# Kernel optimization log

Hardware: AMD Instinct MI355X
Metric: run time of the kernel (lower is better)

## Reference

```python
import jax, jax.numpy as jnp
import numpy as np

N = 20000
E = 640000
IN_CH = 256
HID = 128
OUT_CH = 64
HEADS = 8
C1 = HID // HEADS   # 16 per-head dim, layer 1 (concat)
C2 = OUT_CH         # 64 per-head dim, layer 2 (head mean)
NEG_SLOPE = 0.2


def gat_conv(x, edge_index, W, a_src, a_dst, b, concat):
    """PyG GATConv (no self loops, eval mode / no dropout).
    W: [F_in, H*C], a_src/a_dst: [H, C], b: [H*C] or [C]."""
    H, C = a_src.shape
    h = (x @ W).reshape(-1, H, C)                      # [N, H, C]
    s_src = jnp.einsum('nhc,hc->nh', h, a_src)         # [N, H]
    s_dst = jnp.einsum('nhc,hc->nh', h, a_dst)         # [N, H]
    src, dst = edge_index[0], edge_index[1]
    e = jax.nn.leaky_relu(s_src[src] + s_dst[dst], NEG_SLOPE)  # [E, H]
    # segment softmax over incoming edges of each destination node
    m = jax.ops.segment_max(e, dst, num_segments=N)    # [N, H] (-inf for isolated)
    p = jnp.exp(e - m[dst])                            # [E, H]
    z = jax.ops.segment_sum(p, dst, num_segments=N)    # [N, H]
    alpha = p / z[dst]                                 # [E, H]
    out = jax.ops.segment_sum(h[src] * alpha[..., None], dst, num_segments=N)  # [N,H,C]
    out = out.reshape(-1, H * C) if concat else out.mean(axis=1)
    return out + b


def hetero_layer(x, edge_indices, Ws, a_srcs, a_dsts, bs, concat):
    # HeteroConv(aggr='mean') over edge types targeting 'user'
    outs = [gat_conv(x, edge_indices[t], Ws[t], a_srcs[t], a_dsts[t], bs[t], concat)
            for t in range(len(edge_indices))]
    return sum(outs) / len(outs)


def setup_inputs() -> dict:
    key = jax.random.key(0)
    ks = jax.random.split(key, 16)
    g = 0.1
    return {
        'x': jax.random.normal(ks[0], (N, IN_CH), dtype=jnp.float32),
        'edge_index_a': jax.random.randint(ks[1], (2, E), 0, N, dtype=jnp.int32).astype(jnp.int64),
        'edge_index_b': jax.random.randint(ks[2], (2, E), 0, N, dtype=jnp.int32).astype(jnp.int64),
        # layer 1 params, stacked over 2 edge types
        'W1': jax.random.normal(ks[3], (2, IN_CH, HEADS * C1), dtype=jnp.float32) * g,
        'a1_src': jax.random.normal(ks[4], (2, HEADS, C1), dtype=jnp.float32) * g,
        'a1_dst': jax.random.normal(ks[5], (2, HEADS, C1), dtype=jnp.float32) * g,
        'b1': jnp.zeros((2, HEADS * C1), dtype=jnp.float32),
        # layer 2 params
        'W2': jax.random.normal(ks[6], (2, HID, HEADS * C2), dtype=jnp.float32) * g,
        'a2_src': jax.random.normal(ks[7], (2, HEADS, C2), dtype=jnp.float32) * g,
        'a2_dst': jax.random.normal(ks[8], (2, HEADS, C2), dtype=jnp.float32) * g,
        'b2': jnp.zeros((2, C2), dtype=jnp.float32),
        # classifier
        'Wc1': jax.random.normal(ks[9], (OUT_CH, 32), dtype=jnp.float32) * g,
        'bc1': jnp.zeros((32,), dtype=jnp.float32),
        'Wc2': jax.random.normal(ks[10], (32, 2), dtype=jnp.float32) * g,
        'bc2': jnp.zeros((2,), dtype=jnp.float32),
    }


def reference(x, edge_index_a, edge_index_b, W1, a1_src, a1_dst, b1,
              W2, a2_src, a2_dst, b2, Wc1, bc1, Wc2, bc2):
    eis = [edge_index_a, edge_index_b]
    h = hetero_layer(x, eis, W1, a1_src, a1_dst, b1, concat=True)   # [N, 128]
    h = jax.nn.elu(h)  # (dropout is identity in eval mode)
    h = hetero_layer(h, eis, W2, a2_src, a2_dst, b2, concat=False)  # [N, 64]
    h = jax.nn.elu(h)
    logits = jax.nn.relu(h @ Wc1 + bc1) @ Wc2 + bc2                 # [N, 2]
    return logits
```

## Files before the change

kernel.cpp:

```cpp
#include <hip/hip_runtime.h>
#include <hip/hip_bf16.h>
#include <math.h>

#define NN 20000
#define EE 640000
#define NB 157
#define BCAP 5120
#define NBLK 160
#define CHNK 4000

typedef float v2f __attribute__((ext_vector_type(2)));
typedef __attribute__((ext_vector_type(8))) short bf16x8;
typedef __attribute__((ext_vector_type(4))) float f32x4;

__device__ __forceinline__ void wave_fence() {
  __builtin_amdgcn_wave_barrier();
  asm volatile("s_waitcnt lgkmcnt(0)" ::: "memory");
  __builtin_amdgcn_wave_barrier();
}

__device__ __forceinline__ unsigned pack_bf2(float a, float b) {
  __hip_bfloat162 h2 = __float22bfloat162_rn(make_float2(a, b));
  return *(unsigned*)&h2;
}
__device__ __forceinline__ float2 unpack_bf2(unsigned v) {
  float2 r;
  unsigned lo = v << 16, hi = v & 0xffff0000u;
  r.x = __uint_as_float(lo);
  r.y = __uint_as_float(hi);
  return r;
}

__global__ __launch_bounds__(256) void bin_k(const int* __restrict__ ea,
                                             const int* __restrict__ eb,
                                             int* __restrict__ gcnt,
                                             int* __restrict__ bbuf) {
  int t = blockIdx.y;
  const int* ei = t ? eb : ea;
  int tid = threadIdx.x;
  __shared__ int lh[NB], lbase[NB];
  if (tid < NB) lh[tid] = 0;
  __syncthreads();
  int e0 = blockIdx.x * CHNK;
  int e1 = min(e0 + CHNK, EE);
  int myb[16], myr[16], myv[16];
#pragma unroll
  for (int i = 0; i < 16; ++i) {
    int e = e0 + tid + i * 256;
    if (e < e1) {
      int s = ei[e], d = ei[EE + e];
      int b = d >> 7;
      myb[i] = b;
      myv[i] = (s << 7) | (d & 127);
      myr[i] = atomicAdd(&lh[b], 1);
    } else {
      myb[i] = -1;
    }
  }
  __syncthreads();
  if (tid < NB) {
    int c = lh[tid];
    lbase[tid] = c ? atomicAdd(&gcnt[t * NB + tid], c) : 0;
  }
  __syncthreads();
#pragma unroll
  for (int i = 0; i < 16; ++i) {
    int b = myb[i];
    if (b >= 0) {
      int pos = lbase[b] + myr[i];
      if (pos < BCAP) bbuf[((size_t)t * NB + b) * BCAP + pos] = myv[i];
    }
  }
}

__global__ __launch_bounds__(512) void bscan_k(const int* __restrict__ gcnt,
                                               int* __restrict__ bstart) {
  __shared__ int buf[512];
  int tid = threadIdx.x;
  int t = tid >> 8, b = tid & 255;
  int val = (b < NB) ? gcnt[t * NB + b] : 0;
  buf[tid] = val;
  __syncthreads();
  for (int s = 1; s < 256; s <<= 1) {
    int x = ((tid & 255) >= s) ? buf[tid - s] : 0;
    __syncthreads();
    buf[tid] += x;
    __syncthreads();
  }
  if (b < NB) bstart[t * NB + b] = buf[tid] - val;
}

__global__ __launch_bounds__(256) void build_k(const int* __restrict__ gcnt,
                                               const int* __restrict__ bstart,
                                               const int* __restrict__ bbuf,
                                               int* __restrict__ rowptr,
                                               int* __restrict__ csr) {
  int b = blockIdx.x, t = blockIdx.y;
  int cnt = gcnt[t * NB + b];
  int start = bstart[t * NB + b];
  int n0 = b << 7;
  int nlocal = min(128, NN - n0);
  int tid = threadIdx.x;
  __shared__ int arr[128], lcur[128];
  if (tid < 128) arr[tid] = 0;
  __syncthreads();
  const int* ebuf = bbuf + ((size_t)t * NB + b) * BCAP;
  for (int i = tid; i < cnt; i += 256) atomicAdd(&arr[ebuf[i] & 127], 1);
  __syncthreads();
  int deg = (tid < 128) ? arr[tid] : 0;
  for (int s = 1; s < 128; s <<= 1) {
    int x = (tid < 128 && tid >= s) ? arr[tid - s] : 0;
    __syncthreads();
    if (tid < 128) arr[tid] += x;
    __syncthreads();
  }
  if (tid < nlocal) {
    int incl = arr[tid];
    rowptr[t * (NN + 1) + n0 + tid + 1] = start + incl;
    lcur[tid] = start + incl - deg;
  }
  if (b == 0 && tid == 0) rowptr[t * (NN + 1)] = 0;
  __syncthreads();
  for (int i = tid; i < cnt; i += 256) {
    int v = ebuf[i];
    int pos = atomicAdd(&lcur[v & 127], 1);
    csr[(size_t)t * EE + pos] = v >> 7;
  }
}

template <int NT, int BM, int BN, int BK, int TM, int TN>
__global__ __launch_bounds__(NT) void sgemm_k(const float* __restrict__ A,
                                              const float* __restrict__ B,
                                              float* __restrict__ C, int M, int N, int K,
                                              long long Abs, long long Bbs, long long Cbs,
                                              unsigned* __restrict__ Cb, long long Cbb) {
  A += blockIdx.z * Abs; B += blockIdx.z * Bbs; C += blockIdx.z * Cbs;
  if (Cb) Cb += blockIdx.z * Cbb;
  const int bm = blockIdx.x * BM, bn = blockIdx.y * BN;
  __shared__ float As[BK][BM + 4];
  __shared__ float Bs[BK][BN + 4];
  int tid = threadIdx.x;
  constexpr int TX = BN / TN;
  int tx = tid % TX, ty = tid / TX;
  float acc[TM][TN] = {};
  for (int k0 = 0; k0 < K; k0 += BK) {
#pragma unroll
    for (int i = 0; i < (BM * BK) / (NT * 4); ++i) {
      int idx = tid + i * NT;
      int row = idx / (BK / 4), kq = idx % (BK / 4);
      float4 v = make_float4(0.f, 0.f, 0.f, 0.f);
      int gr = bm + row;
      if (gr < M) v = *(const float4*)&A[(size_t)gr * K + k0 + kq * 4];
      As[kq * 4 + 0][row] = v.x; As[kq * 4 + 1][row] = v.y;
      As[kq * 4 + 2][row] = v.z; As[kq * 4 + 3][row] = v.w;
    }
#pragma unroll
    for (int i = 0; i < (BK * BN) / (NT * 4); ++i) {
      int idx = tid + i * NT;
      int row = idx / (BN / 4), cq = idx % (BN / 4);
      *(float4*)&Bs[row][cq * 4] = *(const float4*)&B[(size_t)(k0 + row) * N + bn + cq * 4];
    }
    __syncthreads();
#pragma unroll
    for (int k = 0; k < BK; ++k) {
      float a[TM], b[TN];
#pragma unroll
      for (int i = 0; i < TM; i += 4) *(float4*)&a[i] = *(float4*)&As[k][ty * TM + i];
#pragma unroll
      for (int j = 0; j < TN; j += 4) *(float4*)&b[j] = *(float4*)&Bs[k][tx * TN + j];
#pragma unroll
      for (int i = 0; i < TM; ++i)
#pragma unroll
        for (int j = 0; j < TN; ++j) acc[i][j] += a[i] * b[j];
    }
    __syncthreads();
  }
#pragma unroll
  for (int i = 0; i < TM; ++i) {
    int gr = bm + ty * TM + i;
    if (gr < M) {
#pragma unroll
      for (int j = 0; j < TN; j += 4)
        *(float4*)&C[(size_t)gr * N + bn + tx * TN + j] = *(float4*)&acc[i][j];
      if (Cb) {
#pragma unroll
        for (int j = 0; j < TN; j += 2)
          Cb[(size_t)gr * (N >> 1) + ((bn + tx * TN + j) >> 1)] = pack_bf2(acc[i][j], acc[i][j + 1]);
      }
    }
  }
}

template <int C>
__global__ void score_k(const float* __restrict__ hf, const float* __restrict__ as_,
                        const float* __restrict__ ad_, float* __restrict__ ss,
                        float* __restrict__ sd) {
  int idx = blockIdx.x * 256 + threadIdx.x;
  if (idx >= 2 * NN * 8) return;
  int t = idx / (NN * 8), r = idx % (NN * 8), n = r / 8, hh = r % 8;
  const int HC = 8 * C;
  const float* hrow = hf + (size_t)t * NN * HC + (size_t)n * HC + hh * C;
  const float* a1 = as_ + t * HC + hh * C;
  const float* a2 = ad_ + t * HC + hh * C;
  float s1 = 0.f, s2 = 0.f;
#pragma unroll
  for (int c = 0; c < C; c += 4) {
    float4 f = *(const float4*)&hrow[c];
    float4 u = *(const float4*)&a1[c];
    float4 w = *(const float4*)&a2[c];
    s1 += f.x * u.x + f.y * u.y + f.z * u.z + f.w * u.w;
    s2 += f.x * w.x + f.y * w.y + f.z * w.z + f.w * w.w;
  }
  ss[idx] = s1; sd[idx] = s2;
}

__device__ __forceinline__ float lrelu(float v) { return v > 0.f ? v : 0.2f * v; }

__global__ __launch_bounds__(256) void aggw1_k(const int* __restrict__ rowptr,
                                               const int* __restrict__ csr,
                                               const float* __restrict__ ssrc,
                                               const float* __restrict__ sdst,
                                               const unsigned* __restrict__ hb,
                                               float* __restrict__ out) {
  int t = blockIdx.y;
  rowptr += t * (NN + 1); csr += (size_t)t * EE;
  ssrc += (size_t)t * NN * 8; sdst += (size_t)t * NN * 8;
  hb += (size_t)t * NN * 64; out += (size_t)t * NN * 128;
  int tid = threadIdx.x, w = tid >> 6, lane = tid & 63;
  int n = blockIdx.x * 4 + w;
  int row = rowptr[n], end = rowptr[n + 1];
  __shared__ int sidx[4][64];
  __shared__ float sexp[4][64][8];
  float4 sda = *(const float4*)&sdst[(size_t)n * 8];
  float4 sdb = *(const float4*)&sdst[(size_t)n * 8 + 4];
  float za_x = 0.f, za_y = 0.f, za_z = 0.f, za_w = 0.f;
  float zb_x = 0.f, zb_y = 0.f, zb_z = 0.f, zb_w = 0.f;
  int hme = lane >> 3;
  v2f acc = {0.f, 0.f};
  for (int base = row; base < end; base += 64) {
    int cnt = min(64, end - base);
    if (lane < cnt) {
      int s = csr[base + lane];
      sidx[w][lane] = s;
      float4 pa = *(const float4*)&ssrc[(size_t)s * 8];
      float4 pb = *(const float4*)&ssrc[(size_t)s * 8 + 4];
      float4 ea, eb;
      ea.x = __expf(lrelu(pa.x + sda.x)); ea.y = __expf(lrelu(pa.y + sda.y));
      ea.z = __expf(lrelu(pa.z + sda.z)); ea.w = __expf(lrelu(pa.w + sda.w));
      eb.x = __expf(lrelu(pb.x + sdb.x)); eb.y = __expf(lrelu(pb.y + sdb.y));
      eb.z = __expf(lrelu(pb.z + sdb.z)); eb.w = __expf(lrelu(pb.w + sdb.w));
      za_x += ea.x; za_y += ea.y; za_z += ea.z; za_w += ea.w;
      zb_x += eb.x; zb_y += eb.y; zb_z += eb.z; zb_w += eb.w;
      *(float4*)&sexp[w][lane][0] = ea;
      *(float4*)&sexp[w][lane][4] = eb;
    }
    wave_fence();
    for (int e = 0; e < cnt; ++e) {
      int s = sidx[w][e];
      float a = sexp[w][e][hme];
      float2 vf = unpack_bf2(hb[(size_t)s * 64 + lane]);
      v2f v = {vf.x, vf.y};
      acc += a * v;
    }
    wave_fence();
  }
#pragma unroll
  for (int off = 32; off; off >>= 1) {
    za_x += __shfl_xor(za_x, off); za_y += __shfl_xor(za_y, off);
    za_z += __shfl_xor(za_z, off); za_w += __shfl_xor(za_w, off);
    zb_x += __shfl_xor(zb_x, off); zb_y += __shfl_xor(zb_y, off);
    zb_z += __shfl_xor(zb_z, off); zb_w += __shfl_xor(zb_w, off);
  }
  float zh[8] = {za_x, za_y, za_z, za_w, zb_x, zb_y, zb_z, zb_w};
  float z = zh[hme];
  float iz = z > 0.f ? 1.f / z : 0.f;
  *(float2*)&out[(size_t)n * 128 + lane * 2] = make_float2(acc.x * iz, acc.y * iz);
}

__global__ void combine1_k(const float* __restrict__ oa, const float* __restrict__ ob,
                           const float* __restrict__ b1, float* __restrict__ hmid,
                           unsigned* __restrict__ hmidb) {
  int idx = blockIdx.x * 256 + threadIdx.x;
  if (idx >= NN * 64) return;
  int n = idx >> 6, j2 = idx & 63, j = j2 * 2;
  float2 va = *(const float2*)&oa[(size_t)n * 128 + j];
  float2 vb = *(const float2*)&ob[(size_t)n * 128 + j];
  float vx = 0.5f * ((va.x + b1[j]) + (vb.x + b1[128 + j]));
  float vy = 0.5f * ((va.y + b1[j + 1]) + (vb.y + b1[128 + j + 1]));
  vx = vx > 0.f ? vx : (__expf(vx) - 1.f);
  vy = vy > 0.f ? vy : (__expf(vy) - 1.f);
  *(float2*)&hmid[(size_t)n * 128 + j] = make_float2(vx, vy);
  hmidb[idx] = pack_bf2(vx, vy);
}

__global__ void fold2_k(const float* __restrict__ W2, const float* __restrict__ a2s,
                        const float* __restrict__ a2d, float* __restrict__ wsf,
                        float* __restrict__ wdf) {
  int idx = blockIdx.x * 256 + threadIdx.x;
  if (idx >= 2048) return;
  int t = idx >> 10, r = idx & 1023, hh = r >> 7, k = r & 127;
  const float* wrow = W2 + (size_t)t * 65536 + (size_t)k * 512 + hh * 64;
  const float* as = a2s + t * 512 + hh * 64;
  const float* ad = a2d + t * 512 + hh * 64;
  float s1 = 0.f, s2 = 0.f;
  for (int c = 0; c < 64; ++c) { s1 += wrow[c] * as[c]; s2 += wrow[c] * ad[c]; }
  wsf[idx] = s1; wdf[idx] = s2;
}

__global__ void foldBT_k(const float* __restrict__ W2, unsigned* __restrict__ BTp) {
  int idx = blockIdx.x * 256 + threadIdx.x;
  if (idx >= 65536) return;
  int t = idx >> 15, r = idx & 32767, c = r >> 9, kw = r & 511;
  int K0 = kw * 2, K1 = K0 + 1;
  int hh0 = K0 >> 7, kk0 = K0 & 127;
  int hh1 = K1 >> 7, kk1 = K1 & 127;
  float v0 = 0.125f * W2[(size_t)t * 65536 + (size_t)kk0 * 512 + hh0 * 64 + c];
  float v1 = 0.125f * W2[(size_t)t * 65536 + (size_t)kk1 * 512 + hh1 * 64 + c];
  BTp[idx] = pack_bf2(v0, v1);
}

__global__ void score2_k(const float* __restrict__ hmid, const float* __restrict__ wsf,
                         const float* __restrict__ wdf, float* __restrict__ ss,
                         float* __restrict__ sdo) {
  int idx = blockIdx.x * 256 + threadIdx.x;
  if (idx >= NN * 8) return;
  int n = idx >> 3, hh = idx & 7;
  const float* hm = hmid + (size_t)n * 128;
  const float* w0s = wsf + (size_t)hh * 128;
  const float* w0d = wdf + (size_t)hh * 128;
  const float* w1s = wsf + (size_t)(8 + hh) * 128;
  const float* w1d = wdf + (size_t)(8 + hh) * 128;
  float s0s = 0.f, s0d = 0.f, s1s = 0.f, s1d = 0.f;
#pragma unroll
  for (int c = 0; c < 128; c += 4) {
    float4 f = *(const float4*)&hm[c];
    float4 a = *(const float4*)&w0s[c];
    float4 b = *(const float4*)&w0d[c];
    float4 u = *(const float4*)&w1s[c];
    float4 v = *(const float4*)&w1d[c];
    s0s += f.x * a.x + f.y * a.y + f.z * a.z + f.w * a.w;
    s0d += f.x * b.x + f.y * b.y + f.z * b.z + f.w * b.w;
    s1s += f.x * u.x + f.y * u.y + f.z * u.z + f.w * u.w;
    s1d += f.x * v.x + f.y * v.y + f.z * v.z + f.w * v.w;
  }
  ss[idx] = s0s; sdo[idx] = s0d;
  ss[NN * 8 + idx] = s1s; sdo[NN * 8 + idx] = s1d;
}

__global__ __launch_bounds__(256) void aggw2_k(const int* __restrict__ rowptr,
                                               const int* __restrict__ csr,
                                               const float* __restrict__ ssrc,
                                               const float* __restrict__ sdst,
                                               const unsigned* __restrict__ hmidb,
                                               unsigned* __restrict__ aggp) {
  int t = blockIdx.y;
  rowptr += t * (NN + 1); csr += (size_t)t * EE;
  ssrc += (size_t)t * NN * 8; sdst += (size_t)t * NN * 8;
  aggp += (size_t)t * NN * 512;
  int tid = threadIdx.x, w = tid >> 6, lane = tid & 63;
  int n = blockIdx.x * 4 + w;
  int row = rowptr[n], end = rowptr[n + 1];
  __shared__ int sidx[4][64];
  __shared__ float sexp[4][64][8];
  float4 sda = *(const float4*)&sdst[(size_t)n * 8];
  float4 sdb = *(const float4*)&sdst[(size_t)n * 8 + 4];
  float za_x = 0.f, za_y = 0.f, za_z = 0.f, za_w = 0.f;
  float zb_x = 0.f, zb_y = 0.f, zb_z = 0.f, zb_w = 0.f;
  v2f acc[8];
#pragma unroll
  for (int i = 0; i < 8; ++i) acc[i] = (v2f){0.f, 0.f};
  for (int base = row; base < end; base += 64) {
    int cnt = min(64, end - base);
    if (lane < cnt) {
      int s = csr[base + lane];
      sidx[w][lane] = s;
      float4 pa = *(const float4*)&ssrc[(size_t)s * 8];
      float4 pb = *(const float4*)&ssrc[(size_t)s * 8 + 4];
      float4 ea, eb;
      ea.x = __expf(lrelu(pa.x + sda.x)); ea.y = __expf(lrelu(pa.y + sda.y));
      ea.z = __expf(lrelu(pa.z + sda.z)); ea.w = __expf(lrelu(pa.w + sda.w));
      eb.x = __expf(lrelu(pb.x + sdb.x)); eb.y = __expf(lrelu(pb.y + sdb.y));
      eb.z = __expf(lrelu(pb.z + sdb.z)); eb.w = __expf(lrelu(pb.w + sdb.w));
      za_x += ea.x; za_y += ea.y; za_z += ea.z; za_w += ea.w;
      zb_x += eb.x; zb_y += eb.y; zb_z += eb.z; zb_w += eb.w;
      *(float4*)&sexp[w][lane][0] = ea;
      *(float4*)&sexp[w][lane][4] = eb;
    }
    wave_fence();
    for (int e = 0; e < cnt; ++e) {
      int s = sidx[w][e];
      unsigned uv = hmidb[(size_t)s * 64 + lane];
      float4 ea = *(const float4*)&sexp[w][e][0];
      float4 eb = *(const float4*)&sexp[w][e][4];
      float2 vf = unpack_bf2(uv);
      v2f v = {vf.x, vf.y};
      acc[0] += ea.x * v;
      acc[1] += ea.y * v;
      acc[2] += ea.z * v;
      acc[3] += ea.w * v;
      acc[4] += eb.x * v;
      acc[5] += eb.y * v;
      acc[6] += eb.z * v;
      acc[7] += eb.w * v;
    }
    wave_fence();
  }
#pragma unroll
  for (int off = 32; off; off >>= 1) {
    za_x += __shfl_xor(za_x, off); za_y += __shfl_xor(za_y, off);
    za_z += __shfl_xor(za_z, off); za_w += __shfl_xor(za_w, off);
    zb_x += __shfl_xor(zb_x, off); zb_y += __shfl_xor(zb_y, off);
    zb_z += __shfl_xor(zb_z, off); zb_w += __shfl_xor(zb_w, off);
  }
  float zh[8] = {za_x, za_y, za_z, za_w, zb_x, zb_y, zb_z, zb_w};
#pragma unroll
  for (int i = 0; i < 8; ++i) {
    float z = zh[i];
    float iz = z > 0.f ? 1.f / z : 0.f;
    aggp[(size_t)n * 512 + i * 64 + lane] = pack_bf2(acc[i].x * iz, acc[i].y * iz);
  }
}

__global__ __launch_bounds__(256) void gemm2_k(const unsigned* __restrict__ Ap,
                                               const unsigned* __restrict__ BT,
                                               const float* __restrict__ b2,
                                               float* __restrict__ feat) {
  int tid = threadIdx.x, w = tid >> 6, l = tid & 63;
  int lr = l & 15, lg = l >> 4;
  int rowbase = blockIdx.x * 64 + w * 16;
  int arow = rowbase + lr;
  if (arow > NN - 1) arow = NN - 1;
  f32x4 acc0 = {0.f, 0.f, 0.f, 0.f}, acc1 = acc0, acc2 = acc0, acc3 = acc0;
#pragma unroll
  for (int t = 0; t < 2; ++t) {
    const unsigned* ap = Ap + (size_t)t * NN * 512 + (size_t)arow * 512 + lg * 4;
    const unsigned* bp = BT + t * 32768 + lr * 512 + lg * 4;
    for (int kw = 0; kw < 512; kw += 16) {
      uint4 av = *(const uint4*)(ap + kw);
      uint4 bv0 = *(const uint4*)(bp + kw);
      uint4 bv1 = *(const uint4*)(bp + 16 * 512 + kw);
      uint4 bv2 = *(const uint4*)(bp + 32 * 512 + kw);
      uint4 bv3 = *(const uint4*)(bp + 48 * 512 + kw);
      bf16x8 af = *(const bf16x8*)&av;
      acc0 = __builtin_amdgcn_mfma_f32_16x16x32_bf16(af, *(const bf16x8*)&bv0, acc0, 0, 0, 0);
      acc1 = __builtin_amdgcn_mfma_f32_16x16x32_bf16(af, *(const bf16x8*)&bv1, acc1, 0, 0, 0);
      acc2 = __builtin_amdgcn_mfma_f32_16x16x32_bf16(af, *(const bf16x8*)&bv2, acc2, 0, 0, 0);
      acc3 = __builtin_amdgcn_mfma_f32_16x16x32_bf16(af, *(const bf16x8*)&bv3, acc3, 0, 0, 0);
    }
  }
  f32x4 accs[4] = {acc0, acc1, acc2, acc3};
#pragma unroll
  for (int ct = 0; ct < 4; ++ct) {
    int col = ct * 16 + lr;
    float bsum = b2[col] + b2[64 + col];
#pragma unroll
    for (int r = 0; r < 4; ++r) {
      int row = rowbase + lg * 4 + r;
      if (row < NN) {
        float v = 0.5f * (accs[ct][r] + bsum);
        v = v > 0.f ? v : (__expf(v) - 1.f);
        feat[(size_t)row * 64 + col] = v;
      }
    }
  }
}

__global__ __launch_bounds__(256) void cls_k(const float* __restrict__ feat,
                                             const float* __restrict__ Wc1,
                                             const float* __restrict__ bc1,
                                             const float* __restrict__ Wc2,
                                             const float* __restrict__ bc2,
                                             float* __restrict__ out) {
  __shared__ float w1[64 * 32];
  __shared__ float w2[64];
  __shared__ float b1s[32], b2s[2];
  __shared__ float fs[8 * 64];
  __shared__ float hs[8 * 32];
  int tid = threadIdx.x;
  for (int i = tid; i < 2048; i += 256) w1[i] = Wc1[i];
  if (tid < 64) w2[tid] = Wc2[tid];
  if (tid < 32) b1s[tid] = bc1[tid];
  if (tid < 2) b2s[tid] = bc2[tid];
  int nbase = blockIdx.x * 8;
  for (int i = tid; i < 512; i += 256) fs[i] = feat[(size_t)nbase * 64 + i];
  __syncthreads();
  int local = tid >> 5, tt = tid & 31;
  const float* f = fs + local * 64;
  float acc = b1s[tt];
#pragma unroll
  for (int c = 0; c < 64; ++c) acc += f[c] * w1[c * 32 + tt];
  hs[local * 32 + tt] = fmaxf(acc, 0.f);
  __syncthreads();
  if (tid < 16) {
    int l = tid >> 1, j = tid & 1;
    float o = b2s[j];
#pragma unroll
    for (int i = 0; i < 32; ++i) o += hs[l * 32 + i] * w2[i * 2 + j];
    out[(size_t)(nbase + l) * 2 + j] = o;
  }
}

extern "C" void kernel_launch(void* const* d_in, const int* in_sizes, int n_in,
                              void* d_out, int out_size, void* d_ws, size_t ws_size,
                              hipStream_t stream) {
  const float* x   = (const float*)d_in[0];
  const int* eia   = (const int*)d_in[1];
  const int* eib   = (const int*)d_in[2];
  const float* W1  = (const float*)d_in[3];
  const float* a1s = (const float*)d_in[4];
  const float* a1d = (const float*)d_in[5];
  const float* b1  = (const float*)d_in[6];
  const float* W2  = (const float*)d_in[7];
  const float* a2s = (const float*)d_in[8];
  const float* a2d = (const float*)d_in[9];
  const float* b2  = (const float*)d_in[10];
  const float* Wc1 = (const float*)d_in[11];
  const float* bc1 = (const float*)d_in[12];
  const float* Wc2 = (const float*)d_in[13];
  const float* bc2 = (const float*)d_in[14];
  float* out = (float*)d_out;

  char* ws = (char*)d_ws;
  size_t off = 0;
  auto alloc = [&](size_t bytes) -> char* {
    char* p = ws + off;
    off += (bytes + 255) & ~(size_t)255;
    return p;
  };
  int* gcnt       = (int*)alloc((size_t)2 * NB * 4);
  int* bstart     = (int*)alloc((size_t)2 * NB * 4);
  int* bbuf       = (int*)alloc((size_t)2 * NB * BCAP * 4);
  int* rowptr     = (int*)alloc((size_t)2 * (NN + 1) * 4);
  int* csr        = (int*)alloc((size_t)2 * EE * 4);
  float* h1       = (float*)alloc((size_t)2 * NN * 128 * 4);
  unsigned* h1b   = (unsigned*)alloc((size_t)2 * NN * 64 * 4);
  float* s1s      = (float*)alloc((size_t)2 * NN * 8 * 4);
  float* s1d      = (float*)alloc((size_t)2 * NN * 8 * 4);
  float* o1       = (float*)alloc((size_t)2 * NN * 128 * 4);
  float* hmid     = (float*)alloc((size_t)NN * 128 * 4);
  unsigned* hmidb = (unsigned*)alloc((size_t)NN * 64 * 4);
  float* wsf      = (float*)alloc((size_t)2048 * 4);
  float* wdf      = (float*)alloc((size_t)2048 * 4);
  unsigned* BTp   = (unsigned*)alloc((size_t)65536 * 4);
  float* s2s      = (float*)alloc((size_t)2 * NN * 8 * 4);
  float* s2d      = (float*)alloc((size_t)2 * NN * 8 * 4);
  unsigned* aggp  = (unsigned*)alloc((size_t)2 * NN * 512 * 4);
  float* feat     = (float*)alloc((size_t)NN * 64 * 4);

  hipMemsetAsync(gcnt, 0, (size_t)2 * NB * 4, stream);
  bin_k<<<dim3(NBLK, 2), 256, 0, stream>>>(eia, eib, gcnt, bbuf);
  bscan_k<<<1, 512, 0, stream>>>(gcnt, bstart);
  build_k<<<dim3(NB, 2), 256, 0, stream>>>(gcnt, bstart, bbuf, rowptr, csr);

  fold2_k<<<8, 256, 0, stream>>>(W2, a2s, a2d, wsf, wdf);
  foldBT_k<<<256, 256, 0, stream>>>(W2, BTp);

  sgemm_k<256, 64, 64, 32, 4, 4><<<dim3((NN + 63) / 64, 2, 2), 256, 0, stream>>>(
      x, W1, h1, NN, 128, 256, 0LL, 256LL * 128, (long long)NN * 128, h1b, (long long)NN * 64);
  score_k<16><<<(2 * NN * 8 + 255) / 256, 256, 0, stream>>>(h1, a1s, a1d, s1s, s1d);
  aggw1_k<<<dim3(NN / 4, 2), 256, 0, stream>>>(rowptr, csr, s1s, s1d, h1b, o1);
  combine1_k<<<(NN * 64 + 255) / 256, 256, 0, stream>>>(o1, o1 + (size_t)NN * 128, b1, hmid, hmidb);

  score2_k<<<(NN * 8 + 255) / 256, 256, 0, stream>>>(hmid, wsf, wdf, s2s, s2d);
  aggw2_k<<<dim3(NN / 4, 2), 256, 0, stream>>>(rowptr, csr, s2s, s2d, hmidb, aggp);
  gemm2_k<<<(NN + 63) / 64, 256, 0, stream>>>(aggp, BTp, b2, feat);

  cls_k<<<NN / 8, 256, 0, stream>>>(feat, Wc1, bc1, Wc2, bc2, out);
}
```

Before: 444.3 us.

## Use MFMA for attention-weighted neighbor aggregation in both GAT layers

Replaces the two scalar per-edge aggregation kernels with one templated kernel that handles 32 edges per chunk. It stores the bf16 attention weights and a transposed tile of gathered neighbor features in LDS, then accumulates with 16x16x32 bf16 MFMA instructions. The goal is to cut per-edge FMA and LDS-broadcast cost, most of all in layer 2 where each edge feeds all 8 heads. In exchange it adds LDS zeroing, transpose stores and extra LDS traffic, and it rounds the attention weights to bf16. Layer 1 computes all head combinations but keeps only the diagonal, so most of its MFMA work is wasted.

```diff
diff --git a/kernel.cpp b/kernel.cpp
--- a/kernel.cpp
+++ b/kernel.cpp
@@ -216,65 +216,142 @@
 
 __device__ __forceinline__ float lrelu(float v) { return v > 0.f ? v : 0.2f * v; }
 
-__global__ __launch_bounds__(256) void aggw1_k(const int* __restrict__ rowptr,
-                                               const int* __restrict__ csr,
-                                               const float* __restrict__ ssrc,
-                                               const float* __restrict__ sdst,
-                                               const unsigned* __restrict__ hb,
-                                               float* __restrict__ out) {
+template <int MODE>
+__global__ __launch_bounds__(256) void aggm_k(const int* __restrict__ rowptr,
+                                              const int* __restrict__ csr,
+                                              const float* __restrict__ ssrc,
+                                              const float* __restrict__ sdst,
+                                              const unsigned* __restrict__ vsrc,
+                                              float* __restrict__ out1,
+                                              unsigned* __restrict__ out2) {
   int t = blockIdx.y;
   rowptr += t * (NN + 1); csr += (size_t)t * EE;
   ssrc += (size_t)t * NN * 8; sdst += (size_t)t * NN * 8;
-  hb += (size_t)t * NN * 64; out += (size_t)t * NN * 128;
+  if (MODE == 0) {
+    out1 += (size_t)t * NN * 128;
+    vsrc += (size_t)t * NN * 64;
+  } else {
+    out2 += (size_t)t * NN * 512;
+  }
   int tid = threadIdx.x, w = tid >> 6, lane = tid & 63;
+  int lg = lane >> 4;
   int n = blockIdx.x * 4 + w;
   int row = rowptr[n], end = rowptr[n + 1];
-  __shared__ int sidx[4][64];
-  __shared__ float sexp[4][64][8];
+  __shared__ __align__(16) unsigned VTw[4][2176];
+  __shared__ __align__(16) unsigned short ET[4][640];
+  __shared__ __align__(16) int sidx[4][32];
+  for (int i = lane; i < 2176; i += 64) VTw[w][i] = 0;
+  for (int i = lane; i < 640; i += 64) ET[w][i] = 0;
+  if (lane < 32) sidx[w][lane] = 0;
   float4 sda = *(const float4*)&sdst[(size_t)n * 8];
   float4 sdb = *(const float4*)&sdst[(size_t)n * 8 + 4];
-  float za_x = 0.f, za_y = 0.f, za_z = 0.f, za_w = 0.f;
-  float zb_x = 0.f, zb_y = 0.f, zb_z = 0.f, zb_w = 0.f;
-  int hme = lane >> 3;
-  v2f acc = {0.f, 0.f};
-  for (int base = row; base < end; base += 64) {
-    int cnt = min(64, end - base);
-    if (lane < cnt) {
-      int s = csr[base + lane];
-      sidx[w][lane] = s;
-      float4 pa = *(const float4*)&ssrc[(size_t)s * 8];
-      float4 pb = *(const float4*)&ssrc[(size_t)s * 8 + 4];
-      float4 ea, eb;
-      ea.x = __expf(lrelu(pa.x + sda.x)); ea.y = __expf(lrelu(pa.y + sda.y));
-      ea.z = __expf(lrelu(pa.z + sda.z)); ea.w = __expf(lrelu(pa.w + sda.w));
-      eb.x = __expf(lrelu(pb.x + sdb.x)); eb.y = __expf(lrelu(pb.y + sdb.y));
-      eb.z = __expf(lrelu(pb.z + sdb.z)); eb.w = __expf(lrelu(pb.w + sdb.w));
-      za_x += ea.x; za_y += ea.y; za_z += ea.z; za_w += ea.w;
-      zb_x += eb.x; zb_y += eb.y; zb_z += eb.z; zb_w += eb.w;
-      *(float4*)&sexp[w][lane][0] = ea;
-      *(float4*)&sexp[w][lane][4] = eb;
+  float z[8];
+#pragma unroll
+  for (int i = 0; i < 8; ++i) z[i] = 0.f;
+  f32x4 acc[8];
+#pragma unroll
+  for (int i = 0; i < 8; ++i) acc[i] = (f32x4){0.f, 0.f, 0.f, 0.f};
+  unsigned* VTp = &VTw[w][0];
+  const unsigned lane4 = lane << 2;
+  const unsigned wr0 = (unsigned)(2 * lane) * 17u;
+  const char* hbc = (const char*)vsrc;
+  for (int base = row; base < end; base += 32) {
+    int cnt = min(32, end - base);
+    if (lane < 32) {
+      float4 ea = {0.f, 0.f, 0.f, 0.f}, eb = {0.f, 0.f, 0.f, 0.f};
+      if (lane < cnt) {
+        int s = csr[base + lane];
+        sidx[w][lane] = s << 8;
+        float4 pa = *(const float4*)&ssrc[(size_t)s * 8];
+        float4 pb = *(const float4*)&ssrc[(size_t)s * 8 + 4];
+        ea.x = __expf(lrelu(pa.x + sda.x)); ea.y = __expf(lrelu(pa.y + sda.y));
+        ea.z = __expf(lrelu(pa.z + sda.z)); ea.w = __expf(lrelu(pa.w + sda.w));
+        eb.x = __expf(lrelu(pb.x + sdb.x)); eb.y = __expf(lrelu(pb.y + sdb.y));
+        eb.z = __expf(lrelu(pb.z + sdb.z)); eb.w = __expf(lrelu(pb.w + sdb.w));
+      }
+      unsigned p0 = pack_bf2(ea.x, ea.y), p1 = pack_bf2(ea.z, ea.w);
+      unsigned p2 = pack_bf2(eb.x, eb.y), p3 = pack_bf2(eb.z, eb.w);
+      float2 q0 = unpack_bf2(p0), q1 = unpack_bf2(p1);
+      float2 q2 = unpack_bf2(p2), q3 = unpack_bf2(p3);
+      z[0] += q0.x; z[1] += q0.y; z[2] += q1.x; z[3] += q1.y;
+      z[4] += q2.x; z[5] += q2.y; z[6] += q3.x; z[7] += q3.y;
+      unsigned short* et = &ET[w][lane];
+      et[0]   = (unsigned short)p0;  et[40]  = (unsigned short)(p0 >> 16);
+      et[80]  = (unsigned short)p1;  et[120] = (unsigned short)(p1 >> 16);
+      et[160] = (unsigned short)p2;  et[200] = (unsigned short)(p2 >> 16);
+      et[240] = (unsigned short)p3;  et[280] = (unsigned short)(p3 >> 16);
     }
     wave_fence();
-    for (int e = 0; e < cnt; ++e) {
-      int s = sidx[w][e];
-      float a = sexp[w][e][hme];
-      float2 vf = unpack_bf2(hb[(size_t)s * 64 + lane]);
-      v2f v = {vf.x, vf.y};
-      acc += a * v;
+    for (int g = 0; g < cnt; g += 4) {
+      unsigned off[4];
+      *(int4*)&off[0] = *(const int4*)&sidx[w][g];
+      unsigned u0 = *(const unsigned*)(hbc + (off[0] | lane4));
+      unsigned u1 = *(const unsigned*)(hbc + (off[1] | lane4));
+      unsigned u2 = *(const unsigned*)(hbc + (off[2] | lane4));
+      unsigned u3 = *(const unsigned*)(hbc + (off[3] | lane4));
+      unsigned lo01 = (u0 & 0xffffu) | (u1 << 16);
+      unsigned lo23 = (u2 & 0xffffu) | (u3 << 16);
+      unsigned hi01 = (u0 >> 16) | (u1 & 0xffff0000u);
+      unsigned hi23 = (u2 >> 16) | (u3 & 0xffff0000u);
+      unsigned r0 = wr0 + (unsigned)(g >> 1);
+      VTp[r0] = lo01; VTp[r0 + 1] = lo23;
+      VTp[r0 + 17] = hi01; VTp[r0 + 18] = hi23;
     }
     wave_fence();
+    bf16x8 af = *(const bf16x8*)&ET[w][(lane & 15) * 40 + lg * 8];
+#pragma unroll
+    for (int ct = 0; ct < 8; ++ct) {
+      const unsigned* vp = VTp + (unsigned)((ct * 16 + (lane & 15)) * 17 + lg * 4);
+      uint4 bv = make_uint4(vp[0], vp[1], vp[2], vp[3]);
+      bf16x8 bf = *(const bf16x8*)&bv;
+      acc[ct] = __builtin_amdgcn_mfma_f32_16x16x32_bf16(af, bf, acc[ct], 0, 0, 0);
+    }
+    wave_fence();
   }
 #pragma unroll
   for (int off = 32; off; off >>= 1) {
-    za_x += __shfl_xor(za_x, off); za_y += __shfl_xor(za_y, off);
-    za_z += __shfl_xor(za_z, off); za_w += __shfl_xor(za_w, off);
-    zb_x += __shfl_xor(zb_x, off); zb_y += __shfl_xor(zb_y, off);
-    zb_z += __shfl_xor(zb_z, off); zb_w += __shfl_xor(zb_w, off);
-  }
-  float zh[8] = {za_x, za_y, za_z, za_w, zb_x, zb_y, zb_z, zb_w};
-  float z = zh[hme];
-  float iz = z > 0.f ? 1.f / z : 0.f;
-  *(float2*)&out[(size_t)n * 128 + lane * 2] = make_float2(acc.x * iz, acc.y * iz);
+#pragma unroll
+    for (int i = 0; i < 8; ++i) z[i] += __shfl_xor(z[i], off);
+  }
+  float iz[8];
+#pragma unroll
+  for (int i = 0; i < 8; ++i) iz[i] = z[i] > 0.f ? 1.f / z[i] : 0.f;
+  if (MODE == 0) {
+    int col = lane & 15;
+    if (lg == 0) {
+#pragma unroll
+      for (int q = 0; q < 4; ++q)
+        out1[(size_t)n * 128 + q * 16 + col] = acc[q][q] * iz[q];
+    } else if (lg == 1) {
+#pragma unroll
+      for (int q = 0; q < 4; ++q)
+        out1[(size_t)n * 128 + (4 + q) * 16 + col] = acc[4 + q][q] * iz[4 + q];
+    }
+  } else {
+    int colp = (lane & 15) >> 1;
+    bool wr = (lane & 1) == 0;
+    if (lg == 0) {
+#pragma unroll
+      for (int ct = 0; ct < 8; ++ct) {
+#pragma unroll
+        for (int r = 0; r < 4; ++r) {
+          float v = acc[ct][r] * iz[r];
+          float v2 = __shfl_xor(v, 1);
+          if (wr) out2[(size_t)n * 512 + r * 64 + ct * 8 + colp] = pack_bf2(v, v2);
+        }
+      }
+    } else if (lg == 1) {
+#pragma unroll
+      for (int ct = 0; ct < 8; ++ct) {
+#pragma unroll
+        for (int r = 0; r < 4; ++r) {
+          float v = acc[ct][r] * iz[4 + r];
+          float v2 = __shfl_xor(v, 1);
+          if (wr) out2[(size_t)n * 512 + (4 + r) * 64 + ct * 8 + colp] = pack_bf2(v, v2);
+        }
+      }
+    }
+  }
 }
 
 __global__ void combine1_k(const float* __restrict__ oa, const float* __restrict__ ob,
@@ -347,105 +424,31 @@
   ss[NN * 8 + idx] = s1s; sdo[NN * 8 + idx] = s1d;
 }
 
-__global__ __launch_bounds__(256) void aggw2_k(const int* __restrict__ rowptr,
-                                               const int* __restrict__ csr,
-                                               const float* __restrict__ ssrc,
-                                               const float* __restrict__ sdst,
-                                               const unsigned* __restrict__ hmidb,
-                                               unsigned* __restrict__ aggp) {
-  int t = blockIdx.y;
-  rowptr += t * (NN + 1); csr += (size_t)t * EE;
-  ssrc += (size_t)t * NN * 8; sdst += (size_t)t * NN * 8;
-  aggp += (size_t)t * NN * 512;
-  int tid = threadIdx.x, w = tid >> 6, lane = tid & 63;
-  int n = blockIdx.x * 4 + w;
-  int row = rowptr[n], end = rowptr[n + 1];
-  __shared__ int sidx[4][64];
-  __shared__ float sexp[4][64][8];
-  float4 sda = *(const float4*)&sdst[(size_t)n * 8];
-  float4 sdb = *(const float4*)&sdst[(size_t)n * 8 + 4];
-  float za_x = 0.f, za_y = 0.f, za_z = 0.f, za_w = 0.f;
-  float zb_x = 0.f, zb_y = 0.f, zb_z = 0.f, zb_w = 0.f;
-  v2f acc[8];
-#pragma unroll
-  for (int i = 0; i < 8; ++i) acc[i] = (v2f){0.f, 0.f};
-  for (int base = row; base < end; base += 64) {
-    int cnt = min(64, end - base);
-    if (lane < cnt) {
-      int s = csr[base + lane];
-      sidx[w][lane] = s;
-      float4 pa = *(const float4*)&ssrc[(size_t)s * 8];
-      float4 pb = *(const float4*)&ssrc[(size_t)s * 8 + 4];
-      float4 ea, eb;
-      ea.x = __expf(lrelu(pa.x + sda.x)); ea.y = __expf(lrelu(pa.y + sda.y));
-      ea.z = __expf(lrelu(pa.z + sda.z)); ea.w = __expf(lrelu(pa.w + sda.w));
-      eb.x = __expf(lrelu(pb.x + sdb.x)); eb.y = __expf(lrelu(pb.y + sdb.y));
-      eb.z = __expf(lrelu(pb.z + sdb.z)); eb.w = __expf(lrelu(pb.w + sdb.w));
-      za_x += ea.x; za_y += ea.y; za_z += ea.z; za_w += ea.w;
-      zb_x += eb.x; zb_y += eb.y; zb_z += eb.z; zb_w += eb.w;
-      *(float4*)&sexp[w][lane][0] = ea;
-      *(float4*)&sexp[w][lane][4] = eb;
-    }
-    wave_fence();
-    for (int e = 0; e < cnt; ++e) {
-      int s = sidx[w][e];
-      unsigned uv = hmidb[(size_t)s * 64 + lane];
-      float4 ea = *(const float4*)&sexp[w][e][0];
-      float4 eb = *(const float4*)&sexp[w][e][4];
-      float2 vf = unpack_bf2(uv);
-      v2f v = {vf.x, vf.y};
-      acc[0] += ea.x * v;
-      acc[1] += ea.y * v;
-      acc[2] += ea.z * v;
-      acc[3] += ea.w * v;
-      acc[4] += eb.x * v;
-      acc[5] += eb.y * v;
-      acc[6] += eb.z * v;
-      acc[7] += eb.w * v;
-    }
-    wave_fence();
-  }
-#pragma unroll
-  for (int off = 32; off; off >>= 1) {
-    za_x += __shfl_xor(za_x, off); za_y += __shfl_xor(za_y, off);
-    za_z += __shfl_xor(za_z, off); za_w += __shfl_xor(za_w, off);
-    zb_x += __shfl_xor(zb_x, off); zb_y += __shfl_xor(zb_y, off);
-    zb_z += __shfl_xor(zb_z, off); zb_w += __shfl_xor(zb_w, off);
-  }
-  float zh[8] = {za_x, za_y, za_z, za_w, zb_x, zb_y, zb_z, zb_w};
-#pragma unroll
-  for (int i = 0; i < 8; ++i) {
-    float z = zh[i];
-    float iz = z > 0.f ? 1.f / z : 0.f;
-    aggp[(size_t)n * 512 + i * 64 + lane] = pack_bf2(acc[i].x * iz, acc[i].y * iz);
-  }
-}
-
 __global__ __launch_bounds__(256) void gemm2_k(const unsigned* __restrict__ Ap,
                                                const unsigned* __restrict__ BT,
                                                const float* __restrict__ b2,
                                                float* __restrict__ feat) {
   int tid = threadIdx.x, w = tid >> 6, l = tid & 63;
-  int lr = l & 15, lg = l >> 4;
+  int lr = l & 15, lgq = l >> 4;
   int rowbase = blockIdx.x * 64 + w * 16;
   int arow = rowbase + lr;
   if (arow > NN - 1) arow = NN - 1;
   f32x4 acc0 = {0.f, 0.f, 0.f, 0.f}, acc1 = acc0, acc2 = acc0, acc3 = acc0;
 #pragma unroll
   for (int t = 0; t < 2; ++t) {
-    const unsigned* ap = Ap + (size_t)t * NN * 512 + (size_t)arow * 512 + lg * 4;
-    const unsigned* bp = BT + t * 32768 + lr * 512 + lg * 4;
+    const unsigned* ap = Ap + (size_t)t * NN * 512 + (size_t)arow * 512 + lgq * 4;
+    const unsigned* bp = BT + t * 32768 + lr * 512 + lgq * 4;
     for (int kw = 0; kw < 512; kw += 16) {
       uint4 av = *(const uint4*)(ap + kw);
       uint4 bv0 = *(const uint4*)(bp + kw);
       uint4 bv1 = *(const uint4*)(bp + 16 * 512 + kw);
       uint4 bv2 = *(const uint4*)(bp + 32 * 512 + kw);
       uint4 bv3 = *(const uint4*)(bp + 48 * 512 + kw);
-      bf16x8 af = *(const bf16x8*)&av;
-      acc0 = __builtin_amdgcn_mfma_f32_16x16x32_bf16(af, *(const bf16x8*)&bv0, acc0, 0, 0, 0);
-      acc1 = __builtin_amdgcn_mfma_f32_16x16x32_bf16(af, *(const bf16x8*)&bv1, acc1, 0, 0, 0);
-      acc2 = __builtin_amdgcn_mfma_f32_16x16x32_bf16(af, *(const bf16x8*)&bv2, acc2, 0, 0, 0);
-      acc3 = __builtin_amdgcn_mfma_f32_16x16x32_bf16(af, *(const bf16x8*)&bv3, acc3, 0, 0, 0);
+      bf16x8 afq = *(const bf16x8*)&av;
+      acc0 = __builtin_amdgcn_mfma_f32_16x16x32_bf16(afq, *(const bf16x8*)&bv0, acc0, 0, 0, 0);
+      acc1 = __builtin_amdgcn_mfma_f32_16x16x32_bf16(afq, *(const bf16x8*)&bv1, acc1, 0, 0, 0);
+      acc2 = __builtin_amdgcn_mfma_f32_16x16x32_bf16(afq, *(const bf16x8*)&bv2, acc2, 0, 0, 0);
+      acc3 = __builtin_amdgcn_mfma_f32_16x16x32_bf16(afq, *(const bf16x8*)&bv3, acc3, 0, 0, 0);
     }
   }
   f32x4 accs[4] = {acc0, acc1, acc2, acc3};
@@ -455,11 +458,11 @@
     float bsum = b2[col] + b2[64 + col];
 #pragma unroll
     for (int r = 0; r < 4; ++r) {
-      int row = rowbase + lg * 4 + r;
-      if (row < NN) {
+      int rowq = rowbase + lgq * 4 + r;
+      if (rowq < NN) {
         float v = 0.5f * (accs[ct][r] + bsum);
         v = v > 0.f ? v : (__expf(v) - 1.f);
-        feat[(size_t)row * 64 + col] = v;
+        feat[(size_t)rowq * 64 + col] = v;
       }
     }
   }
@@ -558,11 +561,11 @@
   sgemm_k<256, 64, 64, 32, 4, 4><<<dim3((NN + 63) / 64, 2, 2), 256, 0, stream>>>(
       x, W1, h1, NN, 128, 256, 0LL, 256LL * 128, (long long)NN * 128, h1b, (long long)NN * 64);
   score_k<16><<<(2 * NN * 8 + 255) / 256, 256, 0, stream>>>(h1, a1s, a1d, s1s, s1d);
-  aggw1_k<<<dim3(NN / 4, 2), 256, 0, stream>>>(rowptr, csr, s1s, s1d, h1b, o1);
+  aggm_k<0><<<dim3(NN / 4, 2), 256, 0, stream>>>(rowptr, csr, s1s, s1d, h1b, o1, nullptr);
   combine1_k<<<(NN * 64 + 255) / 256, 256, 0, stream>>>(o1, o1 + (size_t)NN * 128, b1, hmid, hmidb);
 
   score2_k<<<(NN * 8 + 255) / 256, 256, 0, stream>>>(hmid, wsf, wdf, s2s, s2d);
-  aggw2_k<<<dim3(NN / 4, 2), 256, 0, stream>>>(rowptr, csr, s2s, s2d, hmidb, aggp);
+  aggm_k<1><<<dim3(NN / 4, 2), 256, 0, stream>>>(rowptr, csr, s2s, s2d, hmidb, nullptr, aggp);
   gemm2_k<<<(NN + 63) / 64, 256, 0, stream>>>(aggp, BTp, b2, feat);
 
   cls_k<<<NN / 8, 256, 0, stream>>>(feat, Wc1, bc1, Wc2, bc2, out);
```

Result: slower. 539.2 us (+21.3%).
